# Optimization experiments

Hardware: AMD Instinct MI355X
Metric: run time of the kernel (lower is better)

Reference implementation:

```python
import jax, jax.numpy as jnp
import numpy as np

HP = 64  # padded height (next pow2 of 56)
WP = 64  # padded width
H, W = 56, 56


def fwht(x):
    """Walsh-Hadamard transform along last axis (n must be power of 2)."""
    n = x.shape[-1]
    h = 1
    while h < n:
        xr = x.reshape(*x.shape[:-1], n // (2 * h), 2 * h)
        a = xr[..., :h]
        b = xr[..., h:]
        x = jnp.concatenate([a + b, a - b], axis=-1).reshape(*x.shape[:-1], n)
        h *= 2
    return x


def fwht_axis(x, axis):
    if axis == -1:
        return fwht(x)
    return jnp.swapaxes(fwht(jnp.swapaxes(x, -1, axis)), -1, axis)


def ifwht_axis(x, axis):
    n = x.shape[axis]
    return fwht_axis(x, axis) / n


def setup_inputs() -> dict:
    key = jax.random.key(0)
    k1, k2, k3, k4 = jax.random.split(key, 4)
    x = jax.random.normal(k1, (64, 128, H, W), dtype=jnp.float32)
    # per-pod 1x1 conv weights (pods, out_ch, in_ch), kaiming-ish scale
    conv_w = jax.random.normal(k2, (2, 128, 128), dtype=jnp.float32) / np.sqrt(128.0)
    v = jax.random.uniform(k3, (2, HP, WP), dtype=jnp.float32)
    T = jax.random.uniform(k4, (2, HP, WP), dtype=jnp.float32) / 10.0
    return {"x": x, "conv_w": conv_w, "v": v, "T": T}


def reference(x, conv_w, v, T):
    # pad spatial dims to power of 2 (pad right/bottom)
    f0 = jnp.pad(x, ((0, 0), (0, 0), (0, HP - H), (0, WP - W)))
    # 2D WHT
    f1 = fwht_axis(f0, -1)
    f2 = fwht_axis(f1, -2)
    # per-pod: elementwise gate v, 1x1 conv, soft-threshold; then sum over pods
    # f3: (P, B, Cin, HP, WP)
    f3 = v[:, None, None, :, :] * f2[None]
    f4 = jnp.einsum('pbihw,poi->pbohw', f3, conv_w)
    thr = jax.nn.relu(T)[:, None, None, :, :]
    f5 = jnp.sign(f4) * jax.nn.relu(jnp.abs(f4) - thr)
    f6 = f5.sum(axis=0)
    # inverse 2D WHT
    f7 = ifwht_axis(f6, -1)
    f8 = ifwht_axis(f7, -2)
    y = f8[..., :H, :W]
    return y + x  # residual
```

## Files before the change

### kernel.cpp

```cpp
#include <hip/hip_runtime.h>

typedef unsigned short u16;
typedef unsigned int u32;
typedef __attribute__((ext_vector_type(8))) __bf16 bf16x8;
typedef __attribute__((ext_vector_type(8))) unsigned short u16x8;
typedef __attribute__((ext_vector_type(4))) float f32x4;

__device__ __forceinline__ u16 f2bf(float f) {
  u32 u = __builtin_bit_cast(u32, f);
  u += 0x7FFFu + ((u >> 16) & 1u);
  return (u16)(u >> 16);
}
__device__ __forceinline__ float bf2f(u16 h) {
  u32 u = ((u32)h) << 16;
  return __builtin_bit_cast(float, u);
}

template <int M>
__device__ __forceinline__ void bfly16(float r[16]) {
#pragma unroll
  for (int j = 0; j < 16; ++j)
    if ((j & M) == 0) {
      float a = r[j], b = r[j | M];
      r[j] = a + b;
      r[j | M] = a - b;
    }
}

__global__ __launch_bounds__(256) void k0_wcat(const float* __restrict__ cw,
                                               u16* __restrict__ wc) {
  int i = blockIdx.x * 256 + threadIdx.x;
  wc[i] = f2bf(cw[i]);
}

__global__ __launch_bounds__(256) void k1_fwht(const float* __restrict__ x,
                                               u16* __restrict__ f2) {
  __shared__ float lds[64 * 68];
  const int t = threadIdx.x;
  const size_t bc = blockIdx.x;
  const float* xp = x + bc * 3136;
  float r[16];
  const int hA = t >> 2, wq = t & 3;
  const bool hok = hA < 56;
#pragma unroll
  for (int c4 = 0; c4 < 4; ++c4) {
    const int w0 = wq * 16 + c4 * 4;
    if (hok && w0 < 56) {
      const float4 v4 = *(const float4*)(xp + hA * 56 + w0);
      r[c4 * 4 + 0] = v4.x; r[c4 * 4 + 1] = v4.y;
      r[c4 * 4 + 2] = v4.z; r[c4 * 4 + 3] = v4.w;
    } else {
      r[c4 * 4 + 0] = 0.f; r[c4 * 4 + 1] = 0.f;
      r[c4 * 4 + 2] = 0.f; r[c4 * 4 + 3] = 0.f;
    }
  }
  bfly16<1>(r); bfly16<2>(r); bfly16<4>(r); bfly16<8>(r);
#pragma unroll
  for (int c4 = 0; c4 < 4; ++c4)
    *(float4*)&lds[hA * 68 + wq * 16 + c4 * 4] =
        make_float4(r[c4 * 4 + 0], r[c4 * 4 + 1], r[c4 * 4 + 2], r[c4 * 4 + 3]);
  __syncthreads();
  const int hg = t >> 4, rB = t & 15;
  float q[16];
#pragma unroll
  for (int k = 0; k < 4; ++k)
#pragma unroll
    for (int d = 0; d < 4; ++d)
      q[k * 4 + d] = lds[(hg * 4 + d) * 68 + k * 16 + rB];
  bfly16<4>(q);
  bfly16<8>(q);
  bfly16<1>(q);
  bfly16<2>(q);
#pragma unroll
  for (int k = 0; k < 4; ++k)
#pragma unroll
    for (int d = 0; d < 4; ++d)
      lds[(hg * 4 + d) * 68 + k * 16 + rB] = q[k * 4 + d];
  __syncthreads();
  const int wC = t & 63, rr = t >> 6;
  float s[16];
#pragma unroll
  for (int j = 0; j < 16; ++j) s[j] = lds[(4 * j + rr) * 68 + wC];
  bfly16<1>(s); bfly16<2>(s); bfly16<4>(s); bfly16<8>(s);
  u16* dst = f2 + (bc << 12);
#pragma unroll
  for (int j = 0; j < 16; ++j) dst[(4 * j + rr) * 64 + wC] = f2bf(s[j]);
}

__global__ __launch_bounds__(256) void k2_mix(u16* __restrict__ fg,
                                              const u16* __restrict__ wc,
                                              const float* __restrict__ vv,
                                              const float* __restrict__ tt) {
  __shared__ u16 bt[64 * 136];
  const int t = threadIdx.x;
  const int b = blockIdx.x >> 6;
  const int p0 = (blockIdx.x & 63) << 6;
  u16* fb = fg + ((size_t)b << 19);
  {
    const int c2 = t & 63, pq = t >> 6;
    const u16* s0 = fb + ((size_t)(2 * c2) << 12) + p0 + 16 * pq;
    u16x8 a0 = *(const u16x8*)(s0);
    u16x8 a1 = *(const u16x8*)(s0 + 8);
    u16x8 b0 = *(const u16x8*)(s0 + 4096);
    u16x8 b1 = *(const u16x8*)(s0 + 4096 + 8);
#pragma unroll
    for (int e = 0; e < 8; ++e)
      *(u32*)&bt[(16 * pq + e) * 136 + 2 * c2] = (u32)a0[e] | ((u32)b0[e] << 16);
#pragma unroll
    for (int e = 0; e < 8; ++e)
      *(u32*)&bt[(16 * pq + 8 + e) * 136 + 2 * c2] = (u32)a1[e] | ((u32)b1[e] << 16);
  }
  __syncthreads();
  const int wv = t >> 6, l = t & 63, lr = l & 15, lq = l >> 4;
  f32x4 acc[2][2][4] = {};
#pragma unroll
  for (int q = 0; q < 4; ++q) {
    bf16x8 af[2][2];
#pragma unroll
    for (int fp = 0; fp < 2; ++fp)
#pragma unroll
      for (int fm = 0; fm < 2; ++fm) {
        const int row = fp * 128 + wv * 32 + fm * 16 + lr;
        af[fp][fm] = __builtin_bit_cast(
            bf16x8, *(const u16x8*)(wc + row * 128 + 32 * q + 8 * lq));
      }
#pragma unroll
    for (int fn = 0; fn < 4; ++fn) {
      const bf16x8 bq = __builtin_bit_cast(
          bf16x8, *(const u16x8*)&bt[(fn * 16 + lr) * 136 + 32 * q + 8 * lq]);
#pragma unroll
      for (int fp = 0; fp < 2; ++fp)
#pragma unroll
        for (int fm = 0; fm < 2; ++fm)
          acc[fp][fm][fn] = __builtin_amdgcn_mfma_f32_16x16x32_bf16(
              af[fp][fm], bq, acc[fp][fm][fn], 0, 0, 0);
    }
  }
#pragma unroll
  for (int fn = 0; fn < 4; ++fn) {
    const int pos = p0 + fn * 16 + lr;
    const float v0 = vv[pos], v1 = vv[4096 + pos];
    const float t0 = fmaxf(tt[pos], 0.f), t1 = fmaxf(tt[4096 + pos], 0.f);
#pragma unroll
    for (int fm = 0; fm < 2; ++fm)
#pragma unroll
      for (int rg = 0; rg < 4; ++rg) {
        const float z0 = v0 * acc[0][fm][fn][rg];
        const float z1 = v1 * acc[1][fm][fn][rg];
        const float s0v = copysignf(fmaxf(fabsf(z0) - t0, 0.f), z0);
        const float s1v = copysignf(fmaxf(fabsf(z1) - t1, 0.f), z1);
        const int o = wv * 32 + fm * 16 + lq * 4 + rg;
        fb[(size_t)o * 4096 + pos] = f2bf(s0v + s1v);
      }
  }
}

__global__ __launch_bounds__(256) void k3_iwht(const u16* __restrict__ g,
                                               const float* __restrict__ x,
                                               float* __restrict__ y) {
  __shared__ float lds[64 * 68];
  const int t = threadIdx.x;
  const size_t bo = blockIdx.x;
  const u16* gp = g + (bo << 12);
  float r[16];
  const int hA = t >> 2, wq = t & 3;
  {
    u16x8 a0 = *(const u16x8*)(gp + hA * 64 + wq * 16);
    u16x8 a1 = *(const u16x8*)(gp + hA * 64 + wq * 16 + 8);
#pragma unroll
    for (int e = 0; e < 8; ++e) {
      r[e] = bf2f(a0[e]);
      r[8 + e] = bf2f(a1[e]);
    }
  }
  bfly16<1>(r); bfly16<2>(r); bfly16<4>(r); bfly16<8>(r);
#pragma unroll
  for (int c4 = 0; c4 < 4; ++c4)
    *(float4*)&lds[hA * 68 + wq * 16 + c4 * 4] =
        make_float4(r[c4 * 4 + 0], r[c4 * 4 + 1], r[c4 * 4 + 2], r[c4 * 4 + 3]);
  __syncthreads();
  const int hg = t >> 4, rB = t & 15;
  float q[16];
#pragma unroll
  for (int k = 0; k < 4; ++k)
#pragma unroll
    for (int d = 0; d < 4; ++d)
      q[k * 4 + d] = lds[(hg * 4 + d) * 68 + k * 16 + rB];
  bfly16<4>(q); bfly16<8>(q); bfly16<1>(q); bfly16<2>(q);
#pragma unroll
  for (int k = 0; k < 4; ++k)
#pragma unroll
    for (int d = 0; d < 4; ++d)
      lds[(hg * 4 + d) * 68 + k * 16 + rB] = q[k * 4 + d];
  __syncthreads();
  const int wC = t & 63, rr = t >> 6;
  float s[16];
#pragma unroll
  for (int j = 0; j < 16; ++j) s[j] = lds[(4 * j + rr) * 68 + wC];
  bfly16<1>(s); bfly16<2>(s); bfly16<4>(s); bfly16<8>(s);
  if (wC < 56) {
#pragma unroll
    for (int j = 0; j < 14; ++j) {
      const int h = 4 * j + rr;
      const size_t idx = bo * 3136 + (size_t)(h * 56 + wC);
      y[idx] = x[idx] + s[j] * (1.f / 4096.f);
    }
  }
}

extern "C" void kernel_launch(void* const* d_in, const int* in_sizes, int n_in,
                              void* d_out, int out_size, void* d_ws, size_t ws_size,
                              hipStream_t stream) {
  const float* x = (const float*)d_in[0];
  const float* cw = (const float*)d_in[1];
  const float* v = (const float*)d_in[2];
  const float* T = (const float*)d_in[3];
  float* y = (float*)d_out;

  u16* f2 = (u16*)d_ws;
  u16* wcat = (u16*)((char*)d_ws + 67108864);

  k0_wcat<<<128, 256, 0, stream>>>(cw, wcat);
  k1_fwht<<<8192, 256, 0, stream>>>(x, f2);
  k2_mix<<<4096, 256, 0, stream>>>(f2, wcat, v, T);
  k3_iwht<<<8192, 256, 0, stream>>>(f2, x, y);
}
```

Before: 133.7 us.

## Store WHT intermediate channel-last so the mix GEMM reads operands directly

The intermediate spectrum moves from a [b][c][pos] layout to [b][pos][c]. The forward and inverse WHT kernels now each handle 8 channels per block and write or read 8-channel vectors. The mix kernel loads its B operand straight from global memory with 16-byte loads and writes its output with packed stores, which removes its LDS transpose stage. The cost is fewer WHT blocks (1024), 8 sequential planes per block with extra barriers, and higher register pressure from holding 16 u16x8 vectors.

```diff
diff --git a/kernel.cpp b/kernel.cpp
--- a/kernel.cpp
+++ b/kernel.cpp
@@ -4,6 +4,7 @@
 typedef unsigned int u32;
 typedef __attribute__((ext_vector_type(8))) __bf16 bf16x8;
 typedef __attribute__((ext_vector_type(8))) unsigned short u16x8;
+typedef __attribute__((ext_vector_type(2))) unsigned int u32x2;
 typedef __attribute__((ext_vector_type(4))) float f32x4;
 
 __device__ __forceinline__ u16 f2bf(float f) {
@@ -37,80 +38,73 @@
                                                u16* __restrict__ f2) {
   __shared__ float lds[64 * 68];
   const int t = threadIdx.x;
-  const size_t bc = blockIdx.x;
-  const float* xp = x + bc * 3136;
-  float r[16];
+  const int b = blockIdx.x >> 4;
+  const int cg = blockIdx.x & 15;
   const int hA = t >> 2, wq = t & 3;
+  const int hg = t >> 4, rB = t & 15;
+  const int wC = t & 63, rr = t >> 6;
   const bool hok = hA < 56;
-#pragma unroll
-  for (int c4 = 0; c4 < 4; ++c4) {
-    const int w0 = wq * 16 + c4 * 4;
-    if (hok && w0 < 56) {
-      const float4 v4 = *(const float4*)(xp + hA * 56 + w0);
-      r[c4 * 4 + 0] = v4.x; r[c4 * 4 + 1] = v4.y;
-      r[c4 * 4 + 2] = v4.z; r[c4 * 4 + 3] = v4.w;
-    } else {
-      r[c4 * 4 + 0] = 0.f; r[c4 * 4 + 1] = 0.f;
-      r[c4 * 4 + 2] = 0.f; r[c4 * 4 + 3] = 0.f;
-    }
-  }
-  bfly16<1>(r); bfly16<2>(r); bfly16<4>(r); bfly16<8>(r);
-#pragma unroll
-  for (int c4 = 0; c4 < 4; ++c4)
-    *(float4*)&lds[hA * 68 + wq * 16 + c4 * 4] =
-        make_float4(r[c4 * 4 + 0], r[c4 * 4 + 1], r[c4 * 4 + 2], r[c4 * 4 + 3]);
-  __syncthreads();
-  const int hg = t >> 4, rB = t & 15;
-  float q[16];
-#pragma unroll
-  for (int k = 0; k < 4; ++k)
-#pragma unroll
-    for (int d = 0; d < 4; ++d)
-      q[k * 4 + d] = lds[(hg * 4 + d) * 68 + k * 16 + rB];
-  bfly16<4>(q);
-  bfly16<8>(q);
-  bfly16<1>(q);
-  bfly16<2>(q);
-#pragma unroll
-  for (int k = 0; k < 4; ++k)
-#pragma unroll
-    for (int d = 0; d < 4; ++d)
-      lds[(hg * 4 + d) * 68 + k * 16 + rB] = q[k * 4 + d];
-  __syncthreads();
-  const int wC = t & 63, rr = t >> 6;
-  float s[16];
-#pragma unroll
-  for (int j = 0; j < 16; ++j) s[j] = lds[(4 * j + rr) * 68 + wC];
-  bfly16<1>(s); bfly16<2>(s); bfly16<4>(s); bfly16<8>(s);
-  u16* dst = f2 + (bc << 12);
-#pragma unroll
-  for (int j = 0; j < 16; ++j) dst[(4 * j + rr) * 64 + wC] = f2bf(s[j]);
+  u16x8 outv[16];
+
+#pragma unroll
+  for (int pp = 0; pp < 8; ++pp) {
+    const float* xp = x + (size_t)(b * 128 + cg * 8 + pp) * 3136;
+    float r[16];
+#pragma unroll
+    for (int c4 = 0; c4 < 4; ++c4) {
+      const int w0 = wq * 16 + c4 * 4;
+      if (hok && w0 < 56) {
+        const float4 v4 = *(const float4*)(xp + hA * 56 + w0);
+        r[c4 * 4 + 0] = v4.x; r[c4 * 4 + 1] = v4.y;
+        r[c4 * 4 + 2] = v4.z; r[c4 * 4 + 3] = v4.w;
+      } else {
+        r[c4 * 4 + 0] = 0.f; r[c4 * 4 + 1] = 0.f;
+        r[c4 * 4 + 2] = 0.f; r[c4 * 4 + 3] = 0.f;
+      }
+    }
+    bfly16<1>(r); bfly16<2>(r); bfly16<4>(r); bfly16<8>(r);
+    if (pp) __syncthreads();
+#pragma unroll
+    for (int c4 = 0; c4 < 4; ++c4)
+      *(float4*)&lds[hA * 68 + wq * 16 + c4 * 4] =
+          make_float4(r[c4 * 4 + 0], r[c4 * 4 + 1], r[c4 * 4 + 2], r[c4 * 4 + 3]);
+    __syncthreads();
+    float q[16];
+#pragma unroll
+    for (int k = 0; k < 4; ++k)
+#pragma unroll
+      for (int d = 0; d < 4; ++d)
+        q[k * 4 + d] = lds[(hg * 4 + d) * 68 + k * 16 + rB];
+    bfly16<4>(q); bfly16<8>(q); bfly16<1>(q); bfly16<2>(q);
+#pragma unroll
+    for (int k = 0; k < 4; ++k)
+#pragma unroll
+      for (int d = 0; d < 4; ++d)
+        lds[(hg * 4 + d) * 68 + k * 16 + rB] = q[k * 4 + d];
+    __syncthreads();
+    float s[16];
+#pragma unroll
+    for (int j = 0; j < 16; ++j) s[j] = lds[(4 * j + rr) * 68 + wC];
+    bfly16<1>(s); bfly16<2>(s); bfly16<4>(s); bfly16<8>(s);
+#pragma unroll
+    for (int j = 0; j < 16; ++j) outv[j][pp] = f2bf(s[j]);
+  }
+  u16* dst = f2 + ((size_t)b << 19) + cg * 8;
+#pragma unroll
+  for (int j = 0; j < 16; ++j) {
+    const int pos = (4 * j + rr) * 64 + wC;
+    *(u16x8*)(dst + (size_t)pos * 128) = outv[j];
+  }
 }
 
 __global__ __launch_bounds__(256) void k2_mix(u16* __restrict__ fg,
                                               const u16* __restrict__ wc,
                                               const float* __restrict__ vv,
                                               const float* __restrict__ tt) {
-  __shared__ u16 bt[64 * 136];
   const int t = threadIdx.x;
   const int b = blockIdx.x >> 6;
   const int p0 = (blockIdx.x & 63) << 6;
   u16* fb = fg + ((size_t)b << 19);
-  {
-    const int c2 = t & 63, pq = t >> 6;
-    const u16* s0 = fb + ((size_t)(2 * c2) << 12) + p0 + 16 * pq;
-    u16x8 a0 = *(const u16x8*)(s0);
-    u16x8 a1 = *(const u16x8*)(s0 + 8);
-    u16x8 b0 = *(const u16x8*)(s0 + 4096);
-    u16x8 b1 = *(const u16x8*)(s0 + 4096 + 8);
-#pragma unroll
-    for (int e = 0; e < 8; ++e)
-      *(u32*)&bt[(16 * pq + e) * 136 + 2 * c2] = (u32)a0[e] | ((u32)b0[e] << 16);
-#pragma unroll
-    for (int e = 0; e < 8; ++e)
-      *(u32*)&bt[(16 * pq + 8 + e) * 136 + 2 * c2] = (u32)a1[e] | ((u32)b1[e] << 16);
-  }
-  __syncthreads();
   const int wv = t >> 6, l = t & 63, lr = l & 15, lq = l >> 4;
   f32x4 acc[2][2][4] = {};
 #pragma unroll
@@ -127,7 +121,8 @@
 #pragma unroll
     for (int fn = 0; fn < 4; ++fn) {
       const bf16x8 bq = __builtin_bit_cast(
-          bf16x8, *(const u16x8*)&bt[(fn * 16 + lr) * 136 + 32 * q + 8 * lq]);
+          bf16x8,
+          *(const u16x8*)(fb + (size_t)(p0 + fn * 16 + lr) * 128 + 32 * q + 8 * lq));
 #pragma unroll
       for (int fp = 0; fp < 2; ++fp)
 #pragma unroll
@@ -136,22 +131,29 @@
               af[fp][fm], bq, acc[fp][fm][fn], 0, 0, 0);
     }
   }
+  __syncthreads();
 #pragma unroll
   for (int fn = 0; fn < 4; ++fn) {
     const int pos = p0 + fn * 16 + lr;
     const float v0 = vv[pos], v1 = vv[4096 + pos];
     const float t0 = fmaxf(tt[pos], 0.f), t1 = fmaxf(tt[4096 + pos], 0.f);
 #pragma unroll
-    for (int fm = 0; fm < 2; ++fm)
+    for (int fm = 0; fm < 2; ++fm) {
+      u16 w[4];
 #pragma unroll
       for (int rg = 0; rg < 4; ++rg) {
         const float z0 = v0 * acc[0][fm][fn][rg];
         const float z1 = v1 * acc[1][fm][fn][rg];
         const float s0v = copysignf(fmaxf(fabsf(z0) - t0, 0.f), z0);
         const float s1v = copysignf(fmaxf(fabsf(z1) - t1, 0.f), z1);
-        const int o = wv * 32 + fm * 16 + lq * 4 + rg;
-        fb[(size_t)o * 4096 + pos] = f2bf(s0v + s1v);
-      }
+        w[rg] = f2bf(s0v + s1v);
+      }
+      const int o = wv * 32 + fm * 16 + lq * 4;
+      u32x2 pk;
+      pk[0] = (u32)w[0] | ((u32)w[1] << 16);
+      pk[1] = (u32)w[2] | ((u32)w[3] << 16);
+      *(u32x2*)(fb + (size_t)pos * 128 + o) = pk;
+    }
   }
 }
 
@@ -160,50 +162,54 @@
                                                float* __restrict__ y) {
   __shared__ float lds[64 * 68];
   const int t = threadIdx.x;
-  const size_t bo = blockIdx.x;
-  const u16* gp = g + (bo << 12);
-  float r[16];
+  const int b = blockIdx.x >> 4;
+  const int og = blockIdx.x & 15;
+  const u16* gb = g + ((size_t)b << 19) + og * 8;
   const int hA = t >> 2, wq = t & 3;
-  {
-    u16x8 a0 = *(const u16x8*)(gp + hA * 64 + wq * 16);
-    u16x8 a1 = *(const u16x8*)(gp + hA * 64 + wq * 16 + 8);
-#pragma unroll
-    for (int e = 0; e < 8; ++e) {
-      r[e] = bf2f(a0[e]);
-      r[8 + e] = bf2f(a1[e]);
-    }
-  }
-  bfly16<1>(r); bfly16<2>(r); bfly16<4>(r); bfly16<8>(r);
-#pragma unroll
-  for (int c4 = 0; c4 < 4; ++c4)
-    *(float4*)&lds[hA * 68 + wq * 16 + c4 * 4] =
-        make_float4(r[c4 * 4 + 0], r[c4 * 4 + 1], r[c4 * 4 + 2], r[c4 * 4 + 3]);
-  __syncthreads();
   const int hg = t >> 4, rB = t & 15;
-  float q[16];
-#pragma unroll
-  for (int k = 0; k < 4; ++k)
-#pragma unroll
-    for (int d = 0; d < 4; ++d)
-      q[k * 4 + d] = lds[(hg * 4 + d) * 68 + k * 16 + rB];
-  bfly16<4>(q); bfly16<8>(q); bfly16<1>(q); bfly16<2>(q);
-#pragma unroll
-  for (int k = 0; k < 4; ++k)
-#pragma unroll
-    for (int d = 0; d < 4; ++d)
-      lds[(hg * 4 + d) * 68 + k * 16 + rB] = q[k * 4 + d];
-  __syncthreads();
   const int wC = t & 63, rr = t >> 6;
-  float s[16];
-#pragma unroll
-  for (int j = 0; j < 16; ++j) s[j] = lds[(4 * j + rr) * 68 + wC];
-  bfly16<1>(s); bfly16<2>(s); bfly16<4>(s); bfly16<8>(s);
-  if (wC < 56) {
-#pragma unroll
-    for (int j = 0; j < 14; ++j) {
-      const int h = 4 * j + rr;
-      const size_t idx = bo * 3136 + (size_t)(h * 56 + wC);
-      y[idx] = x[idx] + s[j] * (1.f / 4096.f);
+  u16x8 inv[16];
+#pragma unroll
+  for (int e = 0; e < 16; ++e)
+    inv[e] = *(const u16x8*)(gb + (size_t)(hA * 64 + wq * 16 + e) * 128);
+
+#pragma unroll
+  for (int pp = 0; pp < 8; ++pp) {
+    float r[16];
+#pragma unroll
+    for (int e = 0; e < 16; ++e) r[e] = bf2f(inv[e][pp]);
+    bfly16<1>(r); bfly16<2>(r); bfly16<4>(r); bfly16<8>(r);
+    if (pp) __syncthreads();
+#pragma unroll
+    for (int c4 = 0; c4 < 4; ++c4)
+      *(float4*)&lds[hA * 68 + wq * 16 + c4 * 4] =
+          make_float4(r[c4 * 4 + 0], r[c4 * 4 + 1], r[c4 * 4 + 2], r[c4 * 4 + 3]);
+    __syncthreads();
+    float q[16];
+#pragma unroll
+    for (int k = 0; k < 4; ++k)
+#pragma unroll
+      for (int d = 0; d < 4; ++d)
+        q[k * 4 + d] = lds[(hg * 4 + d) * 68 + k * 16 + rB];
+    bfly16<4>(q); bfly16<8>(q); bfly16<1>(q); bfly16<2>(q);
+#pragma unroll
+    for (int k = 0; k < 4; ++k)
+#pragma unroll
+      for (int d = 0; d < 4; ++d)
+        lds[(hg * 4 + d) * 68 + k * 16 + rB] = q[k * 4 + d];
+    __syncthreads();
+    float s[16];
+#pragma unroll
+    for (int j = 0; j < 16; ++j) s[j] = lds[(4 * j + rr) * 68 + wC];
+    bfly16<1>(s); bfly16<2>(s); bfly16<4>(s); bfly16<8>(s);
+    if (wC < 56) {
+      const size_t plane = (size_t)(b * 128 + og * 8 + pp) * 3136;
+#pragma unroll
+      for (int j = 0; j < 14; ++j) {
+        const int h = 4 * j + rr;
+        const size_t idx = plane + (size_t)(h * 56 + wC);
+        y[idx] = x[idx] + s[j] * (1.f / 4096.f);
+      }
     }
   }
 }
@@ -221,7 +227,7 @@
   u16* wcat = (u16*)((char*)d_ws + 67108864);
 
   k0_wcat<<<128, 256, 0, stream>>>(cw, wcat);
-  k1_fwht<<<8192, 256, 0, stream>>>(x, f2);
+  k1_fwht<<<1024, 256, 0, stream>>>(x, f2);
   k2_mix<<<4096, 256, 0, stream>>>(f2, wcat, v, T);
-  k3_iwht<<<8192, 256, 0, stream>>>(f2, x, y);
-}
+  k3_iwht<<<1024, 256, 0, stream>>>(f2, x, y);
+}
```

After: 270.2 us. 102% more time.
